# Performance work log

Measured on AMD Instinct MI355X. Metric: run time of the kernel, lower is better.

## Reference

```python
import jax, jax.numpy as jnp
import numpy as np

INV_SCALE = 22.627416997969522  # sqrt(512), divisor as in qk.div(inv_scale_factor)
DROPOUT_P = 0.1
DROPOUT_KEY = 42  # fixed key so the reference is deterministic


def setup_inputs() -> dict:
    key = jax.random.key(0)
    k1, k2, k3 = jax.random.split(key, 3)
    return {
        "in1": jax.random.normal(k1, (4, 4096, 512), dtype=jnp.float32),   # [B, S, d]
        "in2": jax.random.normal(k2, (512, 512), dtype=jnp.float32),       # [K, d]
        "value": jax.random.normal(k3, (512, 4096), dtype=jnp.float32),    # [K, dv] (self.value param)
    }


def reference(in1, in2, value):
    # qk = in1 @ in2^T : [B, S, K]
    qk = jnp.einsum('bsd,kd->bsk', in1, in2)
    scaled_qk = qk / INV_SCALE
    probs = jax.nn.softmax(scaled_qk, axis=-1)
    # dropout with fixed key (training-mode semantics, inverted scaling)
    keep = jax.random.bernoulli(jax.random.key(DROPOUT_KEY), 1.0 - DROPOUT_P, probs.shape)
    dropped = jnp.where(keep, probs / (1.0 - DROPOUT_P), 0.0)
    # output = dropped @ value : [B, S, dv]
    return jnp.einsum('bsk,kv->bsv', dropped, value)
```

## Files before the change

kernel.cpp:

```cpp
#include <hip/hip_runtime.h>
#include <stdint.h>


typedef __bf16 bf16x8 __attribute__((ext_vector_type(8)));
typedef unsigned short u16x8 __attribute__((ext_vector_type(8)));
typedef float f32x4 __attribute__((ext_vector_type(4)));

#define SM_SCALE 4.419417382415922e-02f
#define DROP_SCALE (1.0f / 0.9f)

__device__ __forceinline__ unsigned short f2bf(float f) {
  uint32_t u = __float_as_uint(f);
  uint32_t r = (u + 0x7FFFu + ((u >> 16) & 1u)) >> 16;
  return (unsigned short)r;
}
__device__ __forceinline__ float bf2f(unsigned short h) {
  return __uint_as_float(((uint32_t)h) << 16);
}

__device__ __forceinline__ void async16(const void* g, void* l) {
  __builtin_amdgcn_global_load_lds(
      (__attribute__((address_space(1))) uint32_t*)g,
      (__attribute__((address_space(3))) uint32_t*)l, 16, 0, 0);
}

__device__ __forceinline__ void threefry2x32(uint32_t x0, uint32_t x1,
                                             uint32_t& o0, uint32_t& o1) {
  const uint32_t K0 = 0u, K1 = 42u;
  const uint32_t K2 = K0 ^ K1 ^ 0x1BD11BDAu;
  x0 += K0; x1 += K1;
#define TF_R(rot) { x0 += x1; x1 = (x1 << rot) | (x1 >> (32 - rot)); x1 ^= x0; }
  TF_R(13) TF_R(15) TF_R(26) TF_R(6)  x0 += K1; x1 += K2 + 1u;
  TF_R(17) TF_R(29) TF_R(16) TF_R(24) x0 += K2; x1 += K0 + 2u;
  TF_R(13) TF_R(15) TF_R(26) TF_R(6)  x0 += K0; x1 += K1 + 3u;
  TF_R(17) TF_R(29) TF_R(16) TF_R(24) x0 += K1; x1 += K2 + 4u;
  TF_R(13) TF_R(15) TF_R(26) TF_R(6)  x0 += K2; x1 += K0 + 5u;
#undef TF_R
  o0 = x0; o1 = x1;
}

__device__ __forceinline__ bool drop_keep(uint32_t idx) {
  uint32_t o0, o1;
  threefry2x32(0u, idx, o0, o1);
  uint32_t bits = o0 ^ o1;
  float u = __uint_as_float((bits >> 9) | 0x3f800000u) - 1.0f;
  return u < 0.9f;
}

__global__ __launch_bounds__(256) void k_vt(const float* __restrict__ v,
                                            unsigned short* __restrict__ vt) {
  __shared__ float tile[32][33];
  const int nb = blockIdx.x;
  const int kb = blockIdx.y;
  const int tx = threadIdx.x & 31, ty = threadIdx.x >> 5;
#pragma unroll
  for (int yy = 0; yy < 4; ++yy) {
    int row = ty + yy * 8;
    tile[row][tx] = v[(size_t)(kb * 32 + row) * 4096 + nb * 32 + tx];
  }
  __syncthreads();
#pragma unroll
  for (int yy = 0; yy < 4; ++yy) {
    int row = ty + yy * 8;
    vt[(size_t)(nb * 32 + row) * 512 + kb * 32 + tx] = f2bf(tile[tx][row]);
  }
}

__global__ __launch_bounds__(256) void k_cast(const float* __restrict__ src,
                                              unsigned short* __restrict__ dst,
                                              int n4) {
  int i = blockIdx.x * 256 + threadIdx.x;
  if (i >= n4) return;
  float4 v = reinterpret_cast<const float4*>(src)[i];
  ushort4 h;
  h.x = f2bf(v.x); h.y = f2bf(v.y); h.z = f2bf(v.z); h.w = f2bf(v.w);
  reinterpret_cast<ushort4*>(dst)[i] = h;
}

__global__ __launch_bounds__(512, 4) void k_qk(const float* __restrict__ in1,
                                               const unsigned short* __restrict__ B2,
                                               unsigned short* __restrict__ P) {
  __shared__ unsigned short lB[512][36];
  __shared__ float redm[2][64], reds[2][64];

  const int tid = threadIdx.x;
  const int l = tid & 63, w = tid >> 6;
  const int wr = w >> 1, wc = w & 1;
  const int g = l >> 4, c16 = l & 15;
  const int brow = blockIdx.x * 64;

  f32x4 acc[16] = {};

  for (int kt = 0; kt < 16; ++kt) {
    const int k0 = kt * 32;
#pragma unroll
    for (int i = 0; i < 4; ++i) {
      int c = i * 512 + tid;
      int col = c >> 2, sub = c & 3;
      *reinterpret_cast<u16x8*>(&lB[col][sub * 8]) =
          *reinterpret_cast<const u16x8*>(B2 + (size_t)col * 512 + k0 + sub * 8);
    }
    const int arow = brow + wr * 16 + c16;
    float4 v0 = *reinterpret_cast<const float4*>(in1 + (size_t)arow * 512 + k0 + g * 8);
    float4 v1 = *reinterpret_cast<const float4*>(in1 + (size_t)arow * 512 + k0 + g * 8 + 4);
    bf16x8 ahi, alo;
    {
      float vv[8] = {v0.x, v0.y, v0.z, v0.w, v1.x, v1.y, v1.z, v1.w};
      unsigned short h[8], lo8[8];
#pragma unroll
      for (int e = 0; e < 8; ++e) {
        h[e] = f2bf(vv[e]);
        lo8[e] = f2bf(vv[e] - bf2f(h[e]));
      }
      ahi = *reinterpret_cast<const bf16x8*>(h);
      alo = *reinterpret_cast<const bf16x8*>(lo8);
    }
    __syncthreads();
#pragma unroll
    for (int j = 0; j < 16; ++j) {
      const int col = wc * 256 + j * 16 + c16;
      bf16x8 bh = *reinterpret_cast<const bf16x8*>(&lB[col][g * 8]);
      acc[j] = __builtin_amdgcn_mfma_f32_16x16x32_bf16(ahi, bh, acc[j], 0, 0, 0);
      acc[j] = __builtin_amdgcn_mfma_f32_16x16x32_bf16(alo, bh, acc[j], 0, 0, 0);
    }
    __syncthreads();
  }

  const int rowbase = wr * 16 + g * 4;
  float mx[4] = {-3.4e38f, -3.4e38f, -3.4e38f, -3.4e38f};
#pragma unroll
  for (int j = 0; j < 16; ++j)
#pragma unroll
    for (int r = 0; r < 4; ++r) {
      acc[j][r] *= SM_SCALE;
      mx[r] = fmaxf(mx[r], acc[j][r]);
    }
#pragma unroll
  for (int s = 1; s < 16; s <<= 1)
#pragma unroll
    for (int r = 0; r < 4; ++r) mx[r] = fmaxf(mx[r], __shfl_xor(mx[r], s, 64));
  if (c16 == 0) {
#pragma unroll
    for (int r = 0; r < 4; ++r) redm[wc][rowbase + r] = mx[r];
  }
  __syncthreads();
  float rmax[4], sum[4] = {0.f, 0.f, 0.f, 0.f};
#pragma unroll
  for (int r = 0; r < 4; ++r)
    rmax[r] = fmaxf(redm[0][rowbase + r], redm[1][rowbase + r]);
#pragma unroll
  for (int j = 0; j < 16; ++j)
#pragma unroll
    for (int r = 0; r < 4; ++r) {
      float e = expf(acc[j][r] - rmax[r]);
      acc[j][r] = e;
      sum[r] += e;
    }
#pragma unroll
  for (int s = 1; s < 16; s <<= 1)
#pragma unroll
    for (int r = 0; r < 4; ++r) sum[r] += __shfl_xor(sum[r], s, 64);
  if (c16 == 0) {
#pragma unroll
    for (int r = 0; r < 4; ++r) reds[wc][rowbase + r] = sum[r];
  }
  __syncthreads();
  float scl[4];
#pragma unroll
  for (int r = 0; r < 4; ++r)
    scl[r] = DROP_SCALE / (reds[0][rowbase + r] + reds[1][rowbase + r]);

#pragma unroll
  for (int j = 0; j < 16; ++j) {
    const int col = wc * 256 + j * 16 + c16;
#pragma unroll
    for (int r = 0; r < 4; ++r) {
      uint32_t idx = (uint32_t)(brow + rowbase + r) * 512u + (uint32_t)col;
      float pv = drop_keep(idx) ? acc[j][r] * scl[r] : 0.0f;
      P[idx] = f2bf(pv);
    }
  }
}

__global__ __launch_bounds__(512) void k_pv(const unsigned short* __restrict__ P,
                                            const unsigned short* __restrict__ VT,
                                            float* __restrict__ out) {
  __shared__ unsigned short lds[65536];
  const int tid = threadIdx.x;
  const int l = tid & 63, w = tid >> 6;
  const int wr = w >> 2, wc = w & 3;
  const int g = l >> 4, c16 = l & 15;

  const int bid = blockIdx.x;
  const int x = (bid & 7) * 128 + (bid >> 3);
  const int brow = (x >> 4) * 256;
  const int bcol = (x & 15) * 256;

  const int lr_base = w * 16 + (l >> 2);
  const int p = l & 3;

  f32x4 acc[8][4] = {};

#define STAGE(t, kh, b)                                                        \
  {                                                                            \
    const int kofs = (t) * 64 + (kh) * 32;                                     \
    _Pragma("unroll")                                                          \
    for (int i = 0; i < 2; ++i) {                                              \
      int lr = i * 128 + lr_base;                                              \
      int gs = p ^ ((lr >> 1) & 3);                                            \
      unsigned short* dA = lds + ((b) * 2 + (kh)) * 8192 + (i * 512 + w * 64) * 8; \
      async16(P + (size_t)(brow + lr) * 512 + kofs + gs * 8, dA);              \
      async16(VT + (size_t)(bcol + lr) * 512 + kofs + gs * 8, dA + 32768);     \
    }                                                                          \
  }

#define FRAGS(b, kh)                                                           \
  const unsigned short* rbase = lds + ((b) * 2 + (kh)) * 8192;                 \
  bf16x8 a[8], bb[4];                                                          \
  _Pragma("unroll")                                                            \
  for (int mi = 0; mi < 8; ++mi) {                                             \
    int ar = wr * 128 + mi * 16 + c16;                                         \
    a[mi] = *reinterpret_cast<const bf16x8*>(rbase + ar * 32 +                 \
                                             (g ^ ((ar >> 1) & 3)) * 8);       \
  }                                                                            \
  _Pragma("unroll")                                                            \
  for (int nj = 0; nj < 4; ++nj) {                                             \
    int br = wc * 64 + nj * 16 + c16;                                          \
    bb[nj] = *reinterpret_cast<const bf16x8*>(rbase + 32768 + br * 32 +        \
                                              (g ^ ((br >> 1) & 3)) * 8);      \
  }

#define MFMA32()                                                               \
  __builtin_amdgcn_s_setprio(1);                                               \
  _Pragma("unroll")                                                            \
  for (int mi = 0; mi < 8; ++mi)                                               \
    _Pragma("unroll")                                                          \
    for (int nj = 0; nj < 4; ++nj)                                             \
      acc[mi][nj] = __builtin_amdgcn_mfma_f32_16x16x32_bf16(a[mi], bb[nj],     \
                                                            acc[mi][nj], 0, 0, 0); \
  __builtin_amdgcn_s_setprio(0);

  STAGE(0, 0, 0) STAGE(0, 1, 0) STAGE(1, 0, 1)

  for (int t = 0; t < 7; ++t) {
    const int cur = t & 1, nxt = cur ^ 1;
    asm volatile("s_waitcnt vmcnt(8)" ::: "memory");
    __builtin_amdgcn_s_barrier();
    STAGE(t + 1, 1, nxt)
    {
      FRAGS(cur, 0)
      MFMA32()
    }
    asm volatile("s_waitcnt vmcnt(8)" ::: "memory");
    __builtin_amdgcn_s_barrier();
    if (t < 6) STAGE(t + 2, 0, cur)
    {
      FRAGS(cur, 1)
      MFMA32()
    }
  }
  asm volatile("s_waitcnt vmcnt(4)" ::: "memory");
  __builtin_amdgcn_s_barrier();
  {
    FRAGS(1, 0)
    MFMA32()
  }
  asm volatile("s_waitcnt vmcnt(0)" ::: "memory");
  __builtin_amdgcn_s_barrier();
  {
    FRAGS(1, 1)
    MFMA32()
  }
#undef STAGE
#undef FRAGS
#undef MFMA32

#pragma unroll
  for (int i = 0; i < 8; ++i)
#pragma unroll
    for (int r = 0; r < 4; ++r) {
      const size_t row = (size_t)(brow + wr * 128 + i * 16 + g * 4 + r);
      float* o = out + row * 4096 + bcol + wc * 64 + c16;
#pragma unroll
      for (int j = 0; j < 4; ++j) o[j * 16] = acc[i][j][r];
    }
}

extern "C" void kernel_launch(void* const* d_in, const int* in_sizes, int n_in,
                              void* d_out, int out_size, void* d_ws, size_t ws_size,
                              hipStream_t stream) {
  (void)in_sizes; (void)n_in; (void)out_size; (void)ws_size;
  const float* in1   = (const float*)d_in[0];
  const float* in2   = (const float*)d_in[1];
  const float* value = (const float*)d_in[2];
  float* out = (float*)d_out;

  unsigned short* vT   = (unsigned short*)d_ws;
  unsigned short* Pb   = vT + 2097152;
  unsigned short* in2b = Pb + 8388608;

  k_vt<<<dim3(128, 16), dim3(256), 0, stream>>>(value, vT);
  k_cast<<<dim3(256), dim3(256), 0, stream>>>(in2, in2b, 65536);
  k_qk<<<dim3(256), dim3(512), 0, stream>>>(in1, in2b, Pb);
  k_pv<<<dim3(1024), dim3(512), 0, stream>>>(Pb, vT, out);
}
```

Before: 168.5 us.

## Split each K-half into two MFMA phases interleaving LDS reads, async loads and barriers

Restructures the second GEMM's inner loop so each 32-wide K step runs as two phases of 16 MFMAs. LDS fragment reads and half of the global-to-LDS async stage are issued before each phase, and extra barriers keep waves in lockstep. This ping-pong style schedule is meant to overlap memory issue with matrix compute and to lower register pressure, since only 8 fragments are live at once instead of 12. The added barriers cost extra synchronisation and could stall waves if the phases are unbalanced.

```diff
diff --git a/kernel.cpp b/kernel.cpp
--- a/kernel.cpp
+++ b/kernel.cpp
@@ -201,44 +201,60 @@
 
   f32x4 acc[8][4] = {};
 
-#define STAGE(t, kh, b)                                                        \
+#define STAGE_I(t, kh, b, i)                                                   \
   {                                                                            \
     const int kofs = (t) * 64 + (kh) * 32;                                     \
-    _Pragma("unroll")                                                          \
-    for (int i = 0; i < 2; ++i) {                                              \
-      int lr = i * 128 + lr_base;                                              \
-      int gs = p ^ ((lr >> 1) & 3);                                            \
-      unsigned short* dA = lds + ((b) * 2 + (kh)) * 8192 + (i * 512 + w * 64) * 8; \
-      async16(P + (size_t)(brow + lr) * 512 + kofs + gs * 8, dA);              \
-      async16(VT + (size_t)(bcol + lr) * 512 + kofs + gs * 8, dA + 32768);     \
-    }                                                                          \
-  }
-
-#define FRAGS(b, kh)                                                           \
-  const unsigned short* rbase = lds + ((b) * 2 + (kh)) * 8192;                 \
-  bf16x8 a[8], bb[4];                                                          \
-  _Pragma("unroll")                                                            \
-  for (int mi = 0; mi < 8; ++mi) {                                             \
-    int ar = wr * 128 + mi * 16 + c16;                                         \
-    a[mi] = *reinterpret_cast<const bf16x8*>(rbase + ar * 32 +                 \
-                                             (g ^ ((ar >> 1) & 3)) * 8);       \
-  }                                                                            \
-  _Pragma("unroll")                                                            \
-  for (int nj = 0; nj < 4; ++nj) {                                             \
-    int br = wc * 64 + nj * 16 + c16;                                          \
-    bb[nj] = *reinterpret_cast<const bf16x8*>(rbase + 32768 + br * 32 +        \
-                                              (g ^ ((br >> 1) & 3)) * 8);      \
-  }
-
-#define MFMA32()                                                               \
-  __builtin_amdgcn_s_setprio(1);                                               \
-  _Pragma("unroll")                                                            \
-  for (int mi = 0; mi < 8; ++mi)                                               \
+    int lr = (i) * 128 + lr_base;                                              \
+    int gs = p ^ ((lr >> 1) & 3);                                              \
+    unsigned short* dA = lds + ((b) * 2 + (kh)) * 8192 + ((i) * 512 + w * 64) * 8; \
+    async16(P + (size_t)(brow + lr) * 512 + kofs + gs * 8, dA);                \
+    async16(VT + (size_t)(bcol + lr) * 512 + kofs + gs * 8, dA + 32768);       \
+  }
+#define STAGE(t, kh, b) STAGE_I(t, kh, b, 0) STAGE_I(t, kh, b, 1)
+
+#define RD_A(dst, mi_)                                                         \
+  {                                                                            \
+    int ar = wr * 128 + (mi_) * 16 + c16;                                      \
+    dst = *reinterpret_cast<const bf16x8*>(rbase + ar * 32 +                   \
+                                           (g ^ ((ar >> 1) & 3)) * 8);         \
+  }
+#define RD_B(dst, nj_)                                                         \
+  {                                                                            \
+    int br = wc * 64 + (nj_) * 16 + c16;                                       \
+    dst = *reinterpret_cast<const bf16x8*>(rbase + 32768 + br * 32 +           \
+                                           (g ^ ((br >> 1) & 3)) * 8);         \
+  }
+
+#define KHALF(b, kh, st_t, st_kh, st_b, do_st)                                 \
+  {                                                                            \
+    const unsigned short* rbase = lds + ((b) * 2 + (kh)) * 8192;               \
+    bf16x8 av[4], bv[4];                                                       \
+    RD_A(av[0], 0) RD_A(av[1], 1) RD_A(av[2], 2) RD_A(av[3], 3)                \
+    RD_B(bv[0], 0) RD_B(bv[1], 1) RD_B(bv[2], 2) RD_B(bv[3], 3)                \
+    if (do_st) STAGE_I(st_t, st_kh, st_b, 0)                                   \
+    __builtin_amdgcn_s_barrier();                                              \
+    __builtin_amdgcn_s_setprio(1);                                             \
     _Pragma("unroll")                                                          \
     for (int nj = 0; nj < 4; ++nj)                                             \
-      acc[mi][nj] = __builtin_amdgcn_mfma_f32_16x16x32_bf16(a[mi], bb[nj],     \
-                                                            acc[mi][nj], 0, 0, 0); \
-  __builtin_amdgcn_s_setprio(0);
+      _Pragma("unroll")                                                        \
+      for (int m2 = 0; m2 < 4; ++m2)                                           \
+        acc[m2][nj] = __builtin_amdgcn_mfma_f32_16x16x32_bf16(av[m2], bv[nj],  \
+                                                              acc[m2][nj], 0, 0, 0); \
+    __builtin_amdgcn_s_setprio(0);                                             \
+    __builtin_amdgcn_s_barrier();                                              \
+    RD_A(av[0], 4) RD_A(av[1], 5) RD_A(av[2], 6) RD_A(av[3], 7)                \
+    if (do_st) STAGE_I(st_t, st_kh, st_b, 1)                                   \
+    __builtin_amdgcn_s_barrier();                                              \
+    __builtin_amdgcn_s_setprio(1);                                             \
+    _Pragma("unroll")                                                          \
+    for (int nj = 0; nj < 4; ++nj)                                             \
+      _Pragma("unroll")                                                        \
+      for (int m2 = 0; m2 < 4; ++m2)                                           \
+        acc[m2 + 4][nj] = __builtin_amdgcn_mfma_f32_16x16x32_bf16(             \
+            av[m2], bv[nj], acc[m2 + 4][nj], 0, 0, 0);                         \
+    __builtin_amdgcn_s_setprio(0);                                             \
+    __builtin_amdgcn_s_barrier();                                              \
+  }
 
   STAGE(0, 0, 0) STAGE(0, 1, 0) STAGE(1, 0, 1)
 
@@ -246,34 +262,22 @@
     const int cur = t & 1, nxt = cur ^ 1;
     asm volatile("s_waitcnt vmcnt(8)" ::: "memory");
     __builtin_amdgcn_s_barrier();
-    STAGE(t + 1, 1, nxt)
-    {
-      FRAGS(cur, 0)
-      MFMA32()
-    }
+    KHALF(cur, 0, t + 1, 1, nxt, 1)
     asm volatile("s_waitcnt vmcnt(8)" ::: "memory");
     __builtin_amdgcn_s_barrier();
-    if (t < 6) STAGE(t + 2, 0, cur)
-    {
-      FRAGS(cur, 1)
-      MFMA32()
-    }
+    KHALF(cur, 1, t + 2, 0, cur, (t < 6))
   }
   asm volatile("s_waitcnt vmcnt(4)" ::: "memory");
   __builtin_amdgcn_s_barrier();
-  {
-    FRAGS(1, 0)
-    MFMA32()
-  }
+  KHALF(1, 0, 0, 0, 0, 0)
   asm volatile("s_waitcnt vmcnt(0)" ::: "memory");
   __builtin_amdgcn_s_barrier();
-  {
-    FRAGS(1, 1)
-    MFMA32()
-  }
+  KHALF(1, 1, 0, 0, 0, 0)
+#undef KHALF
+#undef RD_A
+#undef RD_B
 #undef STAGE
-#undef FRAGS
-#undef MFMA32
+#undef STAGE_I
 
 #pragma unroll
   for (int i = 0; i < 8; ++i)
```

New measurement: 171.1 us. About the same (+1.6%).
